# Kernel tuning notes

Measured on AMD Instinct MI355X. Metric: run time of the kernel, lower is better.

The kernel has to match this reference:

```python
import jax, jax.numpy as jnp
import numpy as np

N_JOINT = 12
INPUT_DIM = 4
BATCH = 524288


def _skew(w):
    z = jnp.zeros((), w.dtype)
    return jnp.stack([jnp.stack([z, -w[2], w[1]]),
                      jnp.stack([w[2], z, -w[0]]),
                      jnp.stack([-w[1], w[0], z])])


def _srodrigues(twist6, q):
    # twist6: (6,) = [rho; omega]; q: (B,) joint values -> (B,4,4) screw exponential
    rho, omega = twist6[:3], twist6[3:]
    wn = jnp.sqrt(jnp.sum(omega * omega) + 1e-12)
    u, ru = omega / wn, rho / wn
    th = q * wn                                   # (B,)
    K = _skew(u)
    K2 = K @ K
    I3 = jnp.eye(3, dtype=twist6.dtype)
    s = jnp.sin(th)[:, None, None]
    c = (1.0 - jnp.cos(th))[:, None, None]
    t = (th - jnp.sin(th))[:, None, None]
    R = I3 + s * K + c * K2                       # (B,3,3) Rodrigues rotation
    G = th[:, None, None] * I3 + c * K + t * K2   # (B,3,3) translation part
    p = G @ ru                                    # (B,3)
    top = jnp.concatenate([R, p[:, :, None]], axis=2)  # (B,3,4)
    bot = jnp.broadcast_to(jnp.array([0.0, 0.0, 0.0, 1.0], twist6.dtype), (q.shape[0], 1, 4))
    return jnp.concatenate([top, bot], axis=1)


def _rpy2r(rpy):
    r, p, y = rpy[0], rpy[1], rpy[2]
    cr, sr = jnp.cos(r), jnp.sin(r)
    cp, sp = jnp.cos(p), jnp.sin(p)
    cy, sy = jnp.cos(y), jnp.sin(y)
    return jnp.stack([
        jnp.stack([cy * cp, cy * sp * sr - sy * cr, cy * sp * cr + sy * sr]),
        jnp.stack([sy * cp, sy * sp * sr + cy * cr, sy * sp * cr - cy * sr]),
        jnp.stack([-sp, cp * sr, cp * cr])])


def _pr2t(p, rpy):
    R = _rpy2r(rpy)
    top = jnp.concatenate([R, p[:, None]], axis=1)          # (3,4)
    bot = jnp.array([[0.0, 0.0, 0.0, 1.0]], dtype=p.dtype)  # (1,4)
    return jnp.concatenate([top, bot], axis=0)


def setup_inputs() -> dict:
    key = jax.random.key(0)
    ks = jax.random.split(key, 16)
    dims = [INPUT_DIM, 16, 32, 64, 32, N_JOINT]
    inp = {"motor_control": jax.random.normal(ks[0], (BATCH, INPUT_DIM), dtype=jnp.float32)}
    for i in range(5):
        fan_in, fan_out = dims[i], dims[i + 1]
        lim = float(np.sqrt(6.0 / (fan_in + fan_out)))
        inp[f"W{i+1}"] = jax.random.uniform(ks[2 * i + 1], (fan_out, fan_in), minval=-lim, maxval=lim, dtype=jnp.float32)
        inp[f"b{i+1}"] = jax.random.uniform(ks[2 * i + 2], (fan_out,), minval=-0.1, maxval=0.1, dtype=jnp.float32)
    inp["twist"] = jax.random.uniform(ks[11], (N_JOINT, 6, 1), minval=-1.0, maxval=1.0, dtype=jnp.float32)
    inp["init_p"] = jax.random.uniform(ks[12], (1, 3, 1), minval=-1.0, maxval=1.0, dtype=jnp.float32)
    inp["init_rpy"] = jax.random.uniform(ks[13], (1, 3, 1), minval=-1.0, maxval=1.0, dtype=jnp.float32)
    return inp


def reference(motor_control, W1, b1, W2, b2, W3, b3, W4, b4, W5, b5, twist, init_p, init_rpy):
    # q_layer MLP (ReLU after every layer, including the last)
    h = jax.nn.relu(motor_control @ W1.T + b1)
    h = jax.nn.relu(h @ W2.T + b2)
    h = jax.nn.relu(h @ W3.T + b3)
    h = jax.nn.relu(h @ W4.T + b4)
    q = jax.nn.relu(h @ W5.T + b5)  # (B, n_joint)
    B = q.shape[0]
    eye4 = jnp.broadcast_to(jnp.eye(4, dtype=q.dtype), (B, 4, 4))

    def step(carry, xs):
        tw, qj = xs
        return carry @ _srodrigues(tw, qj), None

    out, _ = jax.lax.scan(step, eye4, (twist[:, :, 0], q.T))
    T0 = _pr2t(init_p[0, :, 0], init_rpy[0, :, 0])
    return out @ T0
```

## Files before the change

kernel.cpp:

```cpp
#include <hip/hip_runtime.h>
#include <math.h>

#define BATCH 524288
#define NJ 12

typedef _Float16 half4 __attribute__((ext_vector_type(4)));
typedef float f32x4 __attribute__((ext_vector_type(4)));

#define MFMA16(a, b, c) __builtin_amdgcn_mfma_f32_16x16x16f16((a), (b), (c), 0, 0, 0)

__device__ __forceinline__ f32x4 ld4(const float* p) { return *(const f32x4*)p; }

__device__ __forceinline__ void split4(f32x4 v, half4& h, half4& l) {
    half4 hh, ll;
#pragma unroll
    for (int i = 0; i < 4; i++) {
        float x = v[i];
        _Float16 hi = (_Float16)x;
        hh[i] = hi;
        ll[i] = (_Float16)((x - (float)hi) * 2048.0f);
    }
    h = hh; l = ll;
}

__device__ __forceinline__ f32x4 relu4(f32x4 v) {
    f32x4 r;
#pragma unroll
    for (int i = 0; i < 4; i++) r[i] = fmaxf(v[i], 0.0f);
    return r;
}

__global__ void precompute_kernel(const float* __restrict__ twist,
                                  const float* __restrict__ init_p,
                                  const float* __restrict__ init_rpy,
                                  float* __restrict__ ws) {
    int j = threadIdx.x;
    if (j < NJ) {
        float rho0 = twist[j*6+0], rho1 = twist[j*6+1], rho2 = twist[j*6+2];
        float w0   = twist[j*6+3], w1   = twist[j*6+4], w2   = twist[j*6+5];
        float wn = sqrtf(w0*w0 + w1*w1 + w2*w2 + 1e-12f);
        float inv = 1.0f / wn;
        float u0 = w0*inv, u1 = w1*inv, u2 = w2*inv;
        float ru0 = rho0*inv, ru1 = rho1*inv, ru2 = rho2*inv;
        float kru0 = u1*ru2 - u2*ru1;
        float kru1 = u2*ru0 - u0*ru2;
        float kru2 = u0*ru1 - u1*ru0;
        float ud = u0*ru0 + u1*ru1 + u2*ru2;
        float k2ru0 = u0*ud - ru0;
        float k2ru1 = u1*ud - ru1;
        float k2ru2 = u2*ud - ru2;
        float* o = ws + j*20;
        o[0] = wn;  o[1] = u0;  o[2] = u1;  o[3] = u2;
        o[4] = ru0; o[5] = ru1; o[6] = ru2;
        o[7] = kru0; o[8] = kru1; o[9] = kru2;
        o[10] = k2ru0; o[11] = k2ru1; o[12] = k2ru2;
        o[13] = u0*u0; o[14] = u0*u1; o[15] = u0*u2;
        o[16] = u1*u1; o[17] = u1*u2; o[18] = u2*u2;
    } else if (j == NJ) {
        float r = init_rpy[0], p = init_rpy[1], y = init_rpy[2];
        float cr = cosf(r), sr = sinf(r);
        float cp = cosf(p), sp = sinf(p);
        float cy = cosf(y), sy = sinf(y);
        float* o = ws + NJ*20;
        o[0] = cy*cp; o[1] = cy*sp*sr - sy*cr; o[2] = cy*sp*cr + sy*sr;
        o[3] = sy*cp; o[4] = sy*sp*sr + cy*cr; o[5] = sy*sp*cr - cy*sr;
        o[6] = -sp;   o[7] = cp*sr;            o[8] = cp*cr;
        o[9] = init_p[0]; o[10] = init_p[1]; o[11] = init_p[2];
    }
}

__global__ __launch_bounds__(256) void fk_kernel(
    const float* __restrict__ mc,
    const float* __restrict__ W1, const float* __restrict__ b1,
    const float* __restrict__ W2, const float* __restrict__ b2,
    const float* __restrict__ W3, const float* __restrict__ b3,
    const float* __restrict__ W4, const float* __restrict__ b4,
    const float* __restrict__ W5, const float* __restrict__ b5,
    const float* __restrict__ jc,
    float* __restrict__ out) {
    const int tid = threadIdx.x;
    const int wv = tid >> 6, lane = tid & 63;
    const int qd = lane >> 4, l16 = lane & 15;
    const int wave_base = (blockIdx.x * 4 + wv) * 64;

    __shared__ __align__(16) float qbuf[4][64 * 20];

    const half4 HZ = {(_Float16)0, (_Float16)0, (_Float16)0, (_Float16)0};
    const f32x4 FZ = {0.0f, 0.0f, 0.0f, 0.0f};
    const float inv2048 = 1.0f / 2048.0f;

    half4 a1h, a1l;
    {
        f32x4 w = ld4(W1 + l16 * 4);
        half4 h, l; split4(w, h, l);
        a1h = (qd == 0) ? h : HZ;
        a1l = (qd == 0) ? l : HZ;
    }
    half4 a2h[2], a2l[2];
#pragma unroll
    for (int ot = 0; ot < 2; ot++) {
        f32x4 w = ld4(W2 + (ot*16 + l16)*16 + 4*qd);
        split4(w, a2h[ot], a2l[ot]);
    }
    half4 a3h[4][2], a3l[4][2];
#pragma unroll
    for (int ot = 0; ot < 4; ot++)
#pragma unroll
        for (int kc = 0; kc < 2; kc++) {
            f32x4 w = ld4(W3 + (ot*16 + l16)*32 + kc*16 + 4*qd);
            split4(w, a3h[ot][kc], a3l[ot][kc]);
        }
    half4 a4h[2][4], a4l[2][4];
#pragma unroll
    for (int ot = 0; ot < 2; ot++)
#pragma unroll
        for (int kc = 0; kc < 4; kc++) {
            f32x4 w = ld4(W4 + (ot*16 + l16)*64 + kc*16 + 4*qd);
            split4(w, a4h[ot][kc], a4l[ot][kc]);
        }
    half4 a5h[2], a5l[2];
    {
        int r5 = (l16 < 12) ? l16 : 11;
#pragma unroll
        for (int kc = 0; kc < 2; kc++) {
            f32x4 w = ld4(W5 + r5*32 + kc*16 + 4*qd);
            half4 h, l; split4(w, h, l);
            a5h[kc] = (l16 < 12) ? h : HZ;
            a5l[kc] = (l16 < 12) ? l : HZ;
        }
    }

#pragma unroll 1
    for (int e = 0; e < 4; e++) {
        const int ce = wave_base + e*16 + l16;

        f32x4 xv = ld4(mc + (size_t)ce * 4);
        half4 bxh, bxl; split4(xv, bxh, bxl);
        bxh = (qd == 0) ? bxh : HZ;
        bxl = (qd == 0) ? bxl : HZ;
        f32x4 aH = ld4(b1 + 4*qd);
        f32x4 aL = FZ;
        aH = MFMA16(a1h, bxh, aH);
        aL = MFMA16(a1h, bxl, aL);
        aL = MFMA16(a1l, bxh, aL);
        f32x4 g1 = relu4(aH + aL * inv2048);
        half4 g1h, g1l; split4(g1, g1h, g1l);

        half4 g2h[2], g2l[2];
#pragma unroll
        for (int ot = 0; ot < 2; ot++) {
            f32x4 cH = ld4(b2 + ot*16 + 4*qd);
            f32x4 cL = FZ;
            cH = MFMA16(a2h[ot], g1h, cH);
            cL = MFMA16(a2h[ot], g1l, cL);
            cL = MFMA16(a2l[ot], g1h, cL);
            f32x4 g = relu4(cH + cL * inv2048);
            split4(g, g2h[ot], g2l[ot]);
        }

        half4 g3h[4], g3l[4];
#pragma unroll
        for (int ot = 0; ot < 4; ot++) {
            f32x4 cH = ld4(b3 + ot*16 + 4*qd);
            f32x4 cL = FZ;
#pragma unroll
            for (int kc = 0; kc < 2; kc++) {
                cH = MFMA16(a3h[ot][kc], g2h[kc], cH);
                cL = MFMA16(a3h[ot][kc], g2l[kc], cL);
                cL = MFMA16(a3l[ot][kc], g2h[kc], cL);
            }
            f32x4 g = relu4(cH + cL * inv2048);
            split4(g, g3h[ot], g3l[ot]);
        }

        half4 g4h[2], g4l[2];
#pragma unroll
        for (int ot = 0; ot < 2; ot++) {
            f32x4 cH = ld4(b4 + ot*16 + 4*qd);
            f32x4 cL = FZ;
#pragma unroll
            for (int kc = 0; kc < 4; kc++) {
                cH = MFMA16(a4h[ot][kc], g3h[kc], cH);
                cL = MFMA16(a4h[ot][kc], g3l[kc], cL);
                cL = MFMA16(a4l[ot][kc], g3h[kc], cL);
            }
            f32x4 g = relu4(cH + cL * inv2048);
            split4(g, g4h[ot], g4l[ot]);
        }

        {
            f32x4 cH = ld4(b5 + ((qd < 3) ? 4*qd : 8));
            cH = (qd < 3) ? cH : FZ;
            f32x4 cL = FZ;
#pragma unroll
            for (int kc = 0; kc < 2; kc++) {
                cH = MFMA16(a5h[kc], g4h[kc], cH);
                cL = MFMA16(a5h[kc], g4l[kc], cL);
                cL = MFMA16(a5l[kc], g4h[kc], cL);
            }
            f32x4 qv = relu4(cH + cL * inv2048);
            *(f32x4*)&qbuf[wv][(e*16 + l16)*20 + 4*qd] = qv;
        }
    }

    asm volatile("s_waitcnt lgkmcnt(0)" ::: "memory");

    float qq[12];
    {
        f32x4 qa = *(const f32x4*)&qbuf[wv][lane*20 + 0];
        f32x4 qb = *(const f32x4*)&qbuf[wv][lane*20 + 4];
        f32x4 qc = *(const f32x4*)&qbuf[wv][lane*20 + 8];
        qq[0] = qa[0]; qq[1] = qa[1]; qq[2]  = qa[2]; qq[3]  = qa[3];
        qq[4] = qb[0]; qq[5] = qb[1]; qq[6]  = qb[2]; qq[7]  = qb[3];
        qq[8] = qc[0]; qq[9] = qc[1]; qq[10] = qc[2]; qq[11] = qc[3];
    }

    float M00 = 1.f, M01 = 0.f, M02 = 0.f;
    float M10 = 0.f, M11 = 1.f, M12 = 0.f;
    float M20 = 0.f, M21 = 0.f, M22 = 1.f;
    float v0 = 0.f, v1 = 0.f, v2 = 0.f;

#pragma unroll
    for (int j = 0; j < NJ; j++) {
        const float* c = jc + j*20;
        float wn = c[0];
        float u0 = c[1], u1 = c[2], u2 = c[3];
        float ru0 = c[4], ru1 = c[5], ru2 = c[6];
        float kru0 = c[7], kru1 = c[8], kru2 = c[9];
        float k2ru0 = c[10], k2ru1 = c[11], k2ru2 = c[12];
        float uu00 = c[13], uu01 = c[14], uu02 = c[15];
        float uu11 = c[16], uu12 = c[17], uu22 = c[18];

        float th = qq[j] * wn;
        float s = __sinf(th);
        float cth = __cosf(th);
        float cc = 1.0f - cth;
        float t = th - s;

        float R00 = 1.0f + cc*(uu00 - 1.0f);
        float R01 = cc*uu01 - s*u2;
        float R02 = cc*uu02 + s*u1;
        float R10 = cc*uu01 + s*u2;
        float R11 = 1.0f + cc*(uu11 - 1.0f);
        float R12 = cc*uu12 - s*u0;
        float R20 = cc*uu02 - s*u1;
        float R21 = cc*uu12 + s*u0;
        float R22 = 1.0f + cc*(uu22 - 1.0f);

        float p0 = th*ru0 + cc*kru0 + t*k2ru0;
        float p1 = th*ru1 + cc*kru1 + t*k2ru1;
        float p2 = th*ru2 + cc*kru2 + t*k2ru2;

        float n00 = M00*R00 + M01*R10 + M02*R20;
        float n01 = M00*R01 + M01*R11 + M02*R21;
        float n02 = M00*R02 + M01*R12 + M02*R22;
        float n10 = M10*R00 + M11*R10 + M12*R20;
        float n11 = M10*R01 + M11*R11 + M12*R21;
        float n12 = M10*R02 + M11*R12 + M12*R22;
        float n20 = M20*R00 + M21*R10 + M22*R20;
        float n21 = M20*R01 + M21*R11 + M22*R21;
        float n22 = M20*R02 + M21*R12 + M22*R22;
        v0 += M00*p0 + M01*p1 + M02*p2;
        v1 += M10*p0 + M11*p1 + M12*p2;
        v2 += M20*p0 + M21*p1 + M22*p2;
        M00 = n00; M01 = n01; M02 = n02;
        M10 = n10; M11 = n11; M12 = n12;
        M20 = n20; M21 = n21; M22 = n22;
    }

    const float* t0 = jc + NJ*20;
    float A00 = t0[0], A01 = t0[1], A02 = t0[2];
    float A10 = t0[3], A11 = t0[4], A12 = t0[5];
    float A20 = t0[6], A21 = t0[7], A22 = t0[8];
    float P0  = t0[9], P1  = t0[10], P2 = t0[11];

    float F00 = M00*A00 + M01*A10 + M02*A20;
    float F01 = M00*A01 + M01*A11 + M02*A21;
    float F02 = M00*A02 + M01*A12 + M02*A22;
    float F10 = M10*A00 + M11*A10 + M12*A20;
    float F11 = M10*A01 + M11*A11 + M12*A21;
    float F12 = M10*A02 + M11*A12 + M12*A22;
    float F20 = M20*A00 + M21*A10 + M22*A20;
    float F21 = M20*A01 + M21*A11 + M22*A21;
    float F22 = M20*A02 + M21*A12 + M22*A22;
    float Fv0 = M00*P0 + M01*P1 + M02*P2 + v0;
    float Fv1 = M10*P0 + M11*P1 + M12*P2 + v1;
    float Fv2 = M20*P0 + M21*P1 + M22*P2 + v2;

    const int eo = wave_base + lane;
    float4* o4 = (float4*)(out + (size_t)eo * 16);
    o4[0] = make_float4(F00, F01, F02, Fv0);
    o4[1] = make_float4(F10, F11, F12, Fv1);
    o4[2] = make_float4(F20, F21, F22, Fv2);
    o4[3] = make_float4(0.f, 0.f, 0.f, 1.f);
}

extern "C" void kernel_launch(void* const* d_in, const int* in_sizes, int n_in,
                              void* d_out, int out_size, void* d_ws, size_t ws_size,
                              hipStream_t stream) {
    const float* mc      = (const float*)d_in[0];
    const float* W1      = (const float*)d_in[1];
    const float* b1      = (const float*)d_in[2];
    const float* W2      = (const float*)d_in[3];
    const float* b2      = (const float*)d_in[4];
    const float* W3      = (const float*)d_in[5];
    const float* b3      = (const float*)d_in[6];
    const float* W4      = (const float*)d_in[7];
    const float* b4      = (const float*)d_in[8];
    const float* W5      = (const float*)d_in[9];
    const float* b5      = (const float*)d_in[10];
    const float* twist   = (const float*)d_in[11];
    const float* init_p  = (const float*)d_in[12];
    const float* init_rpy= (const float*)d_in[13];
    float* out = (float*)d_out;
    float* ws  = (float*)d_ws;

    precompute_kernel<<<1, 64, 0, stream>>>(twist, init_p, init_rpy, ws);
    fk_kernel<<<BATCH / 256, 256, 0, stream>>>(
        mc, W1, b1, W2, b2, W3, b3, W4, b4, W5, b5, ws, out);
}
```

Before: 148.7 us.

## Pre-split MLP weights into fp16 hi/lo fragments once and stage them in LDS

```diff
diff --git a/kernel.cpp b/kernel.cpp
--- a/kernel.cpp
+++ b/kernel.cpp
@@ -4,7 +4,11 @@
 #define BATCH 524288
 #define NJ 12
 
+#define WOFF 256
+#define BOFF 5632
+
 typedef _Float16 half4 __attribute__((ext_vector_type(4)));
+typedef _Float16 half2t __attribute__((ext_vector_type(2)));
 typedef float f32x4 __attribute__((ext_vector_type(4)));
 
 #define MFMA16(a, b, c) __builtin_amdgcn_mfma_f32_16x16x16f16((a), (b), (c), 0, 0, 0)
@@ -12,30 +16,47 @@
 __device__ __forceinline__ f32x4 ld4(const float* p) { return *(const f32x4*)p; }
 
 __device__ __forceinline__ void split4(f32x4 v, half4& h, half4& l) {
-    half4 hh, ll;
-#pragma unroll
-    for (int i = 0; i < 4; i++) {
-        float x = v[i];
-        _Float16 hi = (_Float16)x;
-        hh[i] = hi;
-        ll[i] = (_Float16)((x - (float)hi) * 2048.0f);
-    }
-    h = hh; l = ll;
-}
-
-__device__ __forceinline__ f32x4 relu4(f32x4 v) {
+    half2t ha = __builtin_bit_cast(half2t, __builtin_amdgcn_cvt_pkrtz(v[0], v[1]));
+    half2t hb = __builtin_bit_cast(half2t, __builtin_amdgcn_cvt_pkrtz(v[2], v[3]));
+    float r0 = (v[0] - (float)ha[0]) * 2048.0f;
+    float r1 = (v[1] - (float)ha[1]) * 2048.0f;
+    float r2 = (v[2] - (float)hb[0]) * 2048.0f;
+    float r3 = (v[3] - (float)hb[1]) * 2048.0f;
+    half2t la = __builtin_bit_cast(half2t, __builtin_amdgcn_cvt_pkrtz(r0, r1));
+    half2t lb = __builtin_bit_cast(half2t, __builtin_amdgcn_cvt_pkrtz(r2, r3));
+    h = half4{ha[0], ha[1], hb[0], hb[1]};
+    l = half4{la[0], la[1], lb[0], lb[1]};
+}
+
+__device__ __forceinline__ f32x4 relu_comb(f32x4 cH, f32x4 cL) {
+    const float inv2048 = 1.0f / 2048.0f;
     f32x4 r;
 #pragma unroll
-    for (int i = 0; i < 4; i++) r[i] = fmaxf(v[i], 0.0f);
+    for (int i = 0; i < 4; i++) r[i] = fmaxf(fmaf(cL[i], inv2048, cH[i]), 0.0f);
     return r;
+}
+
+__device__ __forceinline__ void unpack_frag(uint4 u, half4& h, half4& l) {
+    uint2 a = make_uint2(u.x, u.y), b = make_uint2(u.z, u.w);
+    h = __builtin_bit_cast(half4, a);
+    l = __builtin_bit_cast(half4, b);
 }
 
 __global__ void precompute_kernel(const float* __restrict__ twist,
                                   const float* __restrict__ init_p,
                                   const float* __restrict__ init_rpy,
+                                  const float* __restrict__ W1, const float* __restrict__ b1,
+                                  const float* __restrict__ W2, const float* __restrict__ b2,
+                                  const float* __restrict__ W3, const float* __restrict__ b3,
+                                  const float* __restrict__ W4, const float* __restrict__ b4,
+                                  const float* __restrict__ W5, const float* __restrict__ b5,
                                   float* __restrict__ ws) {
-    int j = threadIdx.x;
-    if (j < NJ) {
+    const int lane = threadIdx.x;
+    const int qd = lane >> 4, l16 = lane & 15;
+    const f32x4 FZ = {0.f, 0.f, 0.f, 0.f};
+
+    if (lane < NJ) {
+        int j = lane;
         float rho0 = twist[j*6+0], rho1 = twist[j*6+1], rho2 = twist[j*6+2];
         float w0   = twist[j*6+3], w1   = twist[j*6+4], w2   = twist[j*6+5];
         float wn = sqrtf(w0*w0 + w1*w1 + w2*w2 + 1e-12f);
@@ -46,17 +67,14 @@
         float kru1 = u2*ru0 - u0*ru2;
         float kru2 = u0*ru1 - u1*ru0;
         float ud = u0*ru0 + u1*ru1 + u2*ru2;
-        float k2ru0 = u0*ud - ru0;
-        float k2ru1 = u1*ud - ru1;
-        float k2ru2 = u2*ud - ru2;
         float* o = ws + j*20;
         o[0] = wn;  o[1] = u0;  o[2] = u1;  o[3] = u2;
         o[4] = ru0; o[5] = ru1; o[6] = ru2;
         o[7] = kru0; o[8] = kru1; o[9] = kru2;
-        o[10] = k2ru0; o[11] = k2ru1; o[12] = k2ru2;
+        o[10] = u0*ud - ru0; o[11] = u1*ud - ru1; o[12] = u2*ud - ru2;
         o[13] = u0*u0; o[14] = u0*u1; o[15] = u0*u2;
         o[16] = u1*u1; o[17] = u1*u2; o[18] = u2*u2;
-    } else if (j == NJ) {
+    } else if (lane == NJ) {
         float r = init_rpy[0], p = init_rpy[1], y = init_rpy[2];
         float cr = cosf(r), sr = sinf(r);
         float cp = cosf(p), sp = sinf(p);
@@ -67,140 +85,151 @@
         o[6] = -sp;   o[7] = cp*sr;            o[8] = cp*cr;
         o[9] = init_p[0]; o[10] = init_p[1]; o[11] = init_p[2];
     }
-}
-
-__global__ __launch_bounds__(256) void fk_kernel(
+
+    uint4* wf = (uint4*)(ws + WOFF);
+    f32x4* bf = (f32x4*)(ws + BOFF);
+
+    auto pack = [&](f32x4 w) -> uint4 {
+        half4 h, l;
+#pragma unroll
+        for (int i = 0; i < 4; i++) {
+            _Float16 hi = (_Float16)w[i];
+            h[i] = hi;
+            l[i] = (_Float16)((w[i] - (float)hi) * 2048.0f);
+        }
+        uint2 uh = __builtin_bit_cast(uint2, h);
+        uint2 ul = __builtin_bit_cast(uint2, l);
+        return make_uint4(uh.x, uh.y, ul.x, ul.y);
+    };
+
+    {
+        f32x4 w = ld4(W1 + l16*4);
+        wf[0*64 + lane] = pack(qd == 0 ? w : FZ);
+    }
+    for (int ot = 0; ot < 2; ot++)
+        wf[(1+ot)*64 + lane] = pack(ld4(W2 + (ot*16 + l16)*16 + 4*qd));
+    for (int ot = 0; ot < 4; ot++)
+        for (int kc = 0; kc < 2; kc++)
+            wf[(3 + ot*2 + kc)*64 + lane] = pack(ld4(W3 + (ot*16 + l16)*32 + kc*16 + 4*qd));
+    for (int ot = 0; ot < 2; ot++)
+        for (int kc = 0; kc < 4; kc++)
+            wf[(11 + ot*4 + kc)*64 + lane] = pack(ld4(W4 + (ot*16 + l16)*64 + kc*16 + 4*qd));
+    {
+        int r5 = (l16 < 12) ? l16 : 11;
+        for (int kc = 0; kc < 2; kc++) {
+            f32x4 w = ld4(W5 + r5*32 + kc*16 + 4*qd);
+            wf[(19+kc)*64 + lane] = pack(l16 < 12 ? w : FZ);
+        }
+    }
+    bf[0*64 + lane] = ld4(b1 + 4*qd);
+    for (int ot = 0; ot < 2; ot++) bf[(1+ot)*64 + lane] = ld4(b2 + ot*16 + 4*qd);
+    for (int ot = 0; ot < 4; ot++) bf[(3+ot)*64 + lane] = ld4(b3 + ot*16 + 4*qd);
+    for (int ot = 0; ot < 2; ot++) bf[(7+ot)*64 + lane] = ld4(b4 + ot*16 + 4*qd);
+    {
+        f32x4 w = ld4(b5 + ((qd < 3) ? 4*qd : 8));
+        bf[9*64 + lane] = (qd < 3) ? w : FZ;
+    }
+}
+
+__global__ __launch_bounds__(256, 4) void fk_kernel(
     const float* __restrict__ mc,
-    const float* __restrict__ W1, const float* __restrict__ b1,
-    const float* __restrict__ W2, const float* __restrict__ b2,
-    const float* __restrict__ W3, const float* __restrict__ b3,
-    const float* __restrict__ W4, const float* __restrict__ b4,
-    const float* __restrict__ W5, const float* __restrict__ b5,
-    const float* __restrict__ jc,
+    const float* __restrict__ ws,
     float* __restrict__ out) {
     const int tid = threadIdx.x;
     const int wv = tid >> 6, lane = tid & 63;
     const int qd = lane >> 4, l16 = lane & 15;
     const int wave_base = (blockIdx.x * 4 + wv) * 64;
 
-    __shared__ __align__(16) float qbuf[4][64 * 20];
+    const uint4* wf = (const uint4*)(ws + WOFF);
+    const f32x4* bf = (const f32x4*)(ws + BOFF);
+
+    __shared__ __align__(16) uint4 wstage[16*64];
+    __shared__ __align__(16) float qbuf[4][64*20];
+
+    {
+        const uint4* src = wf + 3*64;
+        for (int i = tid; i < 16*64; i += 256) wstage[i] = src[i];
+    }
 
     const half4 HZ = {(_Float16)0, (_Float16)0, (_Float16)0, (_Float16)0};
-    const f32x4 FZ = {0.0f, 0.0f, 0.0f, 0.0f};
-    const float inv2048 = 1.0f / 2048.0f;
-
-    half4 a1h, a1l;
-    {
-        f32x4 w = ld4(W1 + l16 * 4);
-        half4 h, l; split4(w, h, l);
-        a1h = (qd == 0) ? h : HZ;
-        a1l = (qd == 0) ? l : HZ;
-    }
-    half4 a2h[2], a2l[2];
-#pragma unroll
-    for (int ot = 0; ot < 2; ot++) {
-        f32x4 w = ld4(W2 + (ot*16 + l16)*16 + 4*qd);
-        split4(w, a2h[ot], a2l[ot]);
-    }
-    half4 a3h[4][2], a3l[4][2];
-#pragma unroll
-    for (int ot = 0; ot < 4; ot++)
-#pragma unroll
-        for (int kc = 0; kc < 2; kc++) {
-            f32x4 w = ld4(W3 + (ot*16 + l16)*32 + kc*16 + 4*qd);
-            split4(w, a3h[ot][kc], a3l[ot][kc]);
-        }
-    half4 a4h[2][4], a4l[2][4];
-#pragma unroll
-    for (int ot = 0; ot < 2; ot++)
-#pragma unroll
-        for (int kc = 0; kc < 4; kc++) {
-            f32x4 w = ld4(W4 + (ot*16 + l16)*64 + kc*16 + 4*qd);
-            split4(w, a4h[ot][kc], a4l[ot][kc]);
-        }
-    half4 a5h[2], a5l[2];
-    {
-        int r5 = (l16 < 12) ? l16 : 11;
-#pragma unroll
-        for (int kc = 0; kc < 2; kc++) {
-            f32x4 w = ld4(W5 + r5*32 + kc*16 + 4*qd);
-            half4 h, l; split4(w, h, l);
-            a5h[kc] = (l16 < 12) ? h : HZ;
-            a5l[kc] = (l16 < 12) ? l : HZ;
-        }
-    }
+    const f32x4 FZ = {0.f, 0.f, 0.f, 0.f};
+
+    half4 a1h, a1l, a2h[2], a2l[2], a5h[2], a5l[2];
+    unpack_frag(wf[0*64 + lane], a1h, a1l);
+    unpack_frag(wf[1*64 + lane], a2h[0], a2l[0]);
+    unpack_frag(wf[2*64 + lane], a2h[1], a2l[1]);
+    unpack_frag(wf[19*64 + lane], a5h[0], a5l[0]);
+    unpack_frag(wf[20*64 + lane], a5h[1], a5l[1]);
+    f32x4 bias1 = bf[0*64 + lane];
+
+    __syncthreads();
+
+    f32x4 xcur = ld4(mc + (size_t)(wave_base + l16) * 4);
 
 #pragma unroll 1
     for (int e = 0; e < 4; e++) {
-        const int ce = wave_base + e*16 + l16;
-
-        f32x4 xv = ld4(mc + (size_t)ce * 4);
-        half4 bxh, bxl; split4(xv, bxh, bxl);
+        f32x4 xnext;
+        if (e < 3) xnext = ld4(mc + (size_t)(wave_base + (e+1)*16 + l16) * 4);
+
+        half4 bxh, bxl; split4(xcur, bxh, bxl);
         bxh = (qd == 0) ? bxh : HZ;
         bxl = (qd == 0) ? bxl : HZ;
-        f32x4 aH = ld4(b1 + 4*qd);
-        f32x4 aL = FZ;
+        f32x4 aH = bias1, aL = FZ;
         aH = MFMA16(a1h, bxh, aH);
         aL = MFMA16(a1h, bxl, aL);
         aL = MFMA16(a1l, bxh, aL);
-        f32x4 g1 = relu4(aH + aL * inv2048);
-        half4 g1h, g1l; split4(g1, g1h, g1l);
+        half4 g1h, g1l; split4(relu_comb(aH, aL), g1h, g1l);
 
         half4 g2h[2], g2l[2];
 #pragma unroll
         for (int ot = 0; ot < 2; ot++) {
-            f32x4 cH = ld4(b2 + ot*16 + 4*qd);
-            f32x4 cL = FZ;
+            f32x4 cH = bf[(1+ot)*64 + lane], cL = FZ;
             cH = MFMA16(a2h[ot], g1h, cH);
             cL = MFMA16(a2h[ot], g1l, cL);
             cL = MFMA16(a2l[ot], g1h, cL);
-            f32x4 g = relu4(cH + cL * inv2048);
-            split4(g, g2h[ot], g2l[ot]);
+            split4(relu_comb(cH, cL), g2h[ot], g2l[ot]);
         }
 
         half4 g3h[4], g3l[4];
 #pragma unroll
         for (int ot = 0; ot < 4; ot++) {
-            f32x4 cH = ld4(b3 + ot*16 + 4*qd);
-            f32x4 cL = FZ;
+            f32x4 cH = bf[(3+ot)*64 + lane], cL = FZ;
 #pragma unroll
             for (int kc = 0; kc < 2; kc++) {
-                cH = MFMA16(a3h[ot][kc], g2h[kc], cH);
-                cL = MFMA16(a3h[ot][kc], g2l[kc], cL);
-                cL = MFMA16(a3l[ot][kc], g2h[kc], cL);
+                half4 wh, wl; unpack_frag(wstage[(ot*2 + kc)*64 + lane], wh, wl);
+                cH = MFMA16(wh, g2h[kc], cH);
+                cL = MFMA16(wh, g2l[kc], cL);
+                cL = MFMA16(wl, g2h[kc], cL);
             }
-            f32x4 g = relu4(cH + cL * inv2048);
-            split4(g, g3h[ot], g3l[ot]);
+            split4(relu_comb(cH, cL), g3h[ot], g3l[ot]);
         }
 
         half4 g4h[2], g4l[2];
 #pragma unroll
         for (int ot = 0; ot < 2; ot++) {
-            f32x4 cH = ld4(b4 + ot*16 + 4*qd);
-            f32x4 cL = FZ;
+            f32x4 cH = bf[(7+ot)*64 + lane], cL = FZ;
 #pragma unroll
             for (int kc = 0; kc < 4; kc++) {
-                cH = MFMA16(a4h[ot][kc], g3h[kc], cH);
-                cL = MFMA16(a4h[ot][kc], g3l[kc], cL);
-                cL = MFMA16(a4l[ot][kc], g3h[kc], cL);
+                half4 wh, wl; unpack_frag(wstage[(8 + ot*4 + kc)*64 + lane], wh, wl);
+                cH = MFMA16(wh, g3h[kc], cH);
+                cL = MFMA16(wh, g3l[kc], cL);
+                cL = MFMA16(wl, g3h[kc], cL);
             }
-            f32x4 g = relu4(cH + cL * inv2048);
-            split4(g, g4h[ot], g4l[ot]);
+            split4(relu_comb(cH, cL), g4h[ot], g4l[ot]);
         }
 
         {
-            f32x4 cH = ld4(b5 + ((qd < 3) ? 4*qd : 8));
-            cH = (qd < 3) ? cH : FZ;
-            f32x4 cL = FZ;
+            f32x4 cH = bf[9*64 + lane], cL = FZ;
 #pragma unroll
             for (int kc = 0; kc < 2; kc++) {
                 cH = MFMA16(a5h[kc], g4h[kc], cH);
                 cL = MFMA16(a5h[kc], g4l[kc], cL);
                 cL = MFMA16(a5l[kc], g4h[kc], cL);
             }
-            f32x4 qv = relu4(cH + cL * inv2048);
+            f32x4 qv = relu_comb(cH, cL);
             *(f32x4*)&qbuf[wv][(e*16 + l16)*20 + 4*qd] = qv;
         }
+        xcur = xnext;
     }
 
     asm volatile("s_waitcnt lgkmcnt(0)" ::: "memory");
@@ -215,6 +244,7 @@
         qq[8] = qc[0]; qq[9] = qc[1]; qq[10] = qc[2]; qq[11] = qc[3];
     }
 
+    const float* jc = ws;
     float M00 = 1.f, M01 = 0.f, M02 = 0.f;
     float M10 = 0.f, M11 = 1.f, M12 = 0.f;
     float M20 = 0.f, M21 = 0.f, M22 = 1.f;
@@ -315,7 +345,7 @@
     float* out = (float*)d_out;
     float* ws  = (float*)d_ws;
 
-    precompute_kernel<<<1, 64, 0, stream>>>(twist, init_p, init_rpy, ws);
-    fk_kernel<<<BATCH / 256, 256, 0, stream>>>(
-        mc, W1, b1, W2, b2, W3, b3, W4, b4, W5, b5, ws, out);
-}
+    precompute_kernel<<<1, 64, 0, stream>>>(twist, init_p, init_rpy,
+                                            W1, b1, W2, b2, W3, b3, W4, b4, W5, b5, ws);
+    fk_kernel<<<BATCH / 256, 256, 0, stream>>>(mc, ws, out);
+}
```

Result: slower. 218.5 us (+47.0%).
